# Kernel tuning notes

Measured on AMD Instinct MI355X. Metric: run time of the kernel, lower is better.

## Reference

```python
import jax, jax.numpy as jnp
import numpy as np

B, T, IN, H, OUT = 32, 1024, 256, 768, 128


def setup_inputs() -> dict:
    key = jax.random.key(0)
    ks = jax.random.split(key, 11)
    s = 0.05
    return {
        "x": jax.random.normal(ks[0], (B, T, IN), dtype=jnp.float32),
        "W_ih0": jax.random.normal(ks[1], (4 * H, IN), dtype=jnp.float32) * s,
        "W_hh0": jax.random.normal(ks[2], (4 * H, H), dtype=jnp.float32) * s,
        "b_ih0": jax.random.normal(ks[3], (4 * H,), dtype=jnp.float32) * s,
        "b_hh0": jax.random.normal(ks[4], (4 * H,), dtype=jnp.float32) * s,
        "W_ih1": jax.random.normal(ks[5], (4 * H, H), dtype=jnp.float32) * s,
        "W_hh1": jax.random.normal(ks[6], (4 * H, H), dtype=jnp.float32) * s,
        "b_ih1": jax.random.normal(ks[7], (4 * H,), dtype=jnp.float32) * s,
        "b_hh1": jax.random.normal(ks[8], (4 * H,), dtype=jnp.float32) * s,
        "W_lin": jax.random.normal(ks[9], (OUT, H), dtype=jnp.float32) * s,
        "b_lin": jax.random.normal(ks[10], (OUT,), dtype=jnp.float32) * s,
    }


def _lstm_layer(x_btd, W_ih, W_hh, b_ih, b_hh):
    # Input-side GEMM for all timesteps at once: [B,T,4H]
    xg = jnp.einsum("btd,gd->btg", x_btd, W_ih) + b_ih + b_hh
    xg = jnp.swapaxes(xg, 0, 1)  # time-major [T,B,4H]
    h0 = jnp.zeros((x_btd.shape[0], W_hh.shape[1]), x_btd.dtype)

    def step(carry, gx):
        h, c = carry
        g = gx + h @ W_hh.T  # [B,4H]
        i, f, gg, o = jnp.split(g, 4, axis=-1)  # PyTorch gate order i,f,g,o
        i, f, o = jax.nn.sigmoid(i), jax.nn.sigmoid(f), jax.nn.sigmoid(o)
        c = f * c + i * jnp.tanh(gg)
        h = o * jnp.tanh(c)
        return (h, c), h

    _, hs = jax.lax.scan(step, (h0, h0), xg)  # hs: [T,B,H]
    return jnp.swapaxes(hs, 0, 1)  # [B,T,H]


def reference(x, W_ih0, W_hh0, b_ih0, b_hh0, W_ih1, W_hh1, b_ih1, b_hh1, W_lin, b_lin):
    h1 = _lstm_layer(x, W_ih0, W_hh0, b_ih0, b_hh0)
    h2 = _lstm_layer(h1, W_ih1, W_hh1, b_ih1, b_hh1)  # eval mode: inter-layer dropout off
    return jnp.einsum("bth,oh->bto", h2, W_lin) + b_lin
```

## Files before the change

kernel.cpp:

```cpp
#include <hip/hip_runtime.h>

#define Tt    1024
#define INF   256
#define Hh    768
#define OUTF  128

#define NWG_L0  48
#define NWG_L1  48
#define NWG_LIN 2
#define NWG     (NWG_L0 + NWG_L1 + NWG_LIN)
#define NTHR    1024

typedef unsigned int       u32;
typedef unsigned long long u64;
typedef unsigned short     u16;
typedef __attribute__((ext_vector_type(8))) short bf16x8;
typedef __attribute__((ext_vector_type(4))) float f32x4;

#define PROG_OFF 0
#define HA_OFF   16384
#define HB_OFF   (HA_OFF + 3*49152)
#define WS_BYTES (HB_OFF + 3*49152)
#define HPS      24576

#define ASTR_B 1552
#define RSLAB  272
#define RROW   17

__device__ __forceinline__ float sigf(float v){ return 1.0f/(1.0f+__expf(-v)); }
__device__ __forceinline__ float tanhfast(float x){
    const float cx = fminf(fmaxf(x, -15.f), 15.f);
    const float e  = __expf(2.f * cx);
    return (e - 1.f) / (e + 1.f);
}
__device__ __forceinline__ u16 f2bf(float f){
    u32 u = __float_as_uint(f);
    return (u16)((u + 0x7fffu + ((u>>16)&1u)) >> 16);
}
__device__ __forceinline__ void st32ws(u16* p, u32 v){
    __hip_atomic_store((u32*)p, v, __ATOMIC_RELAXED, __HIP_MEMORY_SCOPE_AGENT);
}
__device__ __forceinline__ u32 ldu32(const u32* p){
    return __hip_atomic_load(p, __ATOMIC_RELAXED, __HIP_MEMORY_SCOPE_AGENT);
}
__device__ __forceinline__ void stu32(u32* p, u32 v){
    __hip_atomic_store(p, v, __ATOMIC_RELAXED, __HIP_MEMORY_SCOPE_AGENT);
}
__device__ __forceinline__ void ld16x3(const u16* p0, const u16* p1, const u16* p2,
                                       f32x4& r0, f32x4& r1, f32x4& r2){
    asm volatile(
        "global_load_dwordx4 %0, %3, off sc0 sc1\n\t"
        "global_load_dwordx4 %1, %4, off sc0 sc1\n\t"
        "global_load_dwordx4 %2, %5, off sc0 sc1\n\t"
        "s_waitcnt vmcnt(0)"
        : "=&v"(r0), "=&v"(r1), "=&v"(r2)
        : "v"(p0), "v"(p1), "v"(p2)
        : "memory");
}
__device__ __forceinline__ void ld16x6(const u16* p0, const u16* p1, const u16* p2,
                                       const u16* p3, const u16* p4, const u16* p5,
                                       f32x4& r0, f32x4& r1, f32x4& r2,
                                       f32x4& r3, f32x4& r4, f32x4& r5){
    asm volatile(
        "global_load_dwordx4 %0, %6, off sc0 sc1\n\t"
        "global_load_dwordx4 %1, %7, off sc0 sc1\n\t"
        "global_load_dwordx4 %2, %8, off sc0 sc1\n\t"
        "global_load_dwordx4 %3, %9, off sc0 sc1\n\t"
        "global_load_dwordx4 %4, %10, off sc0 sc1\n\t"
        "global_load_dwordx4 %5, %11, off sc0 sc1\n\t"
        "s_waitcnt vmcnt(0)"
        : "=&v"(r0), "=&v"(r1), "=&v"(r2), "=&v"(r3), "=&v"(r4), "=&v"(r5)
        : "v"(p0), "v"(p1), "v"(p2), "v"(p3), "v"(p4), "v"(p5)
        : "memory");
}

__device__ __forceinline__ void waitlines(u32* prog, int base, int cnt, u32 thr, int lane){
    bool ok = (lane >= cnt);
    int guard = 0;
    while (guard < (1 << 24)) {
        if (!ok) ok = (ldu32(prog + (base + lane) * 32) >= thr);
        if (__ballot(ok) == ~0ull) break;
        __builtin_amdgcn_s_sleep(1);
        ++guard;
    }
}

__global__ void prologue(char* ws){
    int i = blockIdx.x * 256 + threadIdx.x;
    if (i < WS_BYTES / 4)
        __hip_atomic_store(((u32*)ws) + i, 0u, __ATOMIC_RELAXED, __HIP_MEMORY_SCOPE_AGENT);
}

__device__ __forceinline__ bf16x8 load8w(const float* p){
    float4 v0 = *(const float4*)(p);
    float4 v1 = *(const float4*)(p + 4);
    bf16x8 r;
    r[0]=(short)f2bf(v0.x); r[1]=(short)f2bf(v0.y); r[2]=(short)f2bf(v0.z); r[3]=(short)f2bf(v0.w);
    r[4]=(short)f2bf(v1.x); r[5]=(short)f2bf(v1.y); r[6]=(short)f2bf(v1.z); r[7]=(short)f2bf(v1.w);
    return r;
}

__global__ __launch_bounds__(NTHR) void lstm_persist(
    const float* __restrict__ x,
    const float* __restrict__ Wih0, const float* __restrict__ Whh0,
    const float* __restrict__ bih0, const float* __restrict__ bhh0,
    const float* __restrict__ Wih1, const float* __restrict__ Whh1,
    const float* __restrict__ bih1, const float* __restrict__ bhh1,
    const float* __restrict__ Wlin, const float* __restrict__ blin,
    float* __restrict__ out, char* ws)
{
    u32* prog = (u32*)(ws + PROG_OFF);
    u16* hA   = (u16*)(ws + HA_OFF);
    u16* hB   = (u16*)(ws + HB_OFF);

    const int wg  = blockIdx.x;
    const int tid = threadIdx.x;

    __shared__ __align__(16) char smem[49664];
    char*  actb = smem;
    float* red  = (float*)smem;

    const int lane = tid & 63, w = tid >> 6;
    const int quad = lane >> 4, nl = lane & 15;
    const int nt = w >> 2, ks = w & 3;
    const int b3 = tid >> 5, q = tid & 31;

    const int role  = (wg < NWG_L0) ? 0 : ((wg < NWG_L0 + NWG_L1) ? 1 : 2);
    const int jbase = (role == 0) ? wg * 16 : ((role == 1) ? (wg - NWG_L0) * 16 : 0);
    const int obase = (role == 2) ? (wg - NWG_L0 - NWG_L1) * 64 : 0;

    bf16x8 bfr[12];
    if (role == 0) {
        const int grow = nt * Hh + jbase + nl;
        #pragma unroll
        for (int fi = 0; fi < 8; ++fi) {
            const int c = fi >> 2, fc = fi & 3;
            const int ka = c * 512 + ks * 128 + fc * 32 + quad * 8;
            const float* p = (ka < 256) ? (Wih0 + (size_t)grow * 256 + ka)
                                        : (Whh0 + (size_t)grow * 768 + (ka - 256));
            bfr[fi] = load8w(p);
        }
    } else if (role == 1) {
        const int grow = nt * Hh + jbase + nl;
        #pragma unroll
        for (int fi = 0; fi < 12; ++fi) {
            const int c = fi / 6, fc = fi % 6;
            const int ka = c * 768 + ks * 192 + fc * 32 + quad * 8;
            const float* p = (ka < 768) ? (Wih1 + (size_t)grow * 768 + ka)
                                        : (Whh1 + (size_t)grow * 768 + (ka - 768));
            bfr[fi] = load8w(p);
        }
    } else {
        const int row = obase + nt * 16 + nl;
        #pragma unroll
        for (int fi = 0; fi < 6; ++fi) {
            const int ka = ks * 192 + fi * 32 + quad * 8;
            bfr[fi] = load8w(Wlin + (size_t)row * 768 + ka);
        }
    }

    float ba0=0,ba1=0,ba2=0,ba3=0, bb0=0,bb1=0,bb2=0,bb3=0, creg0=0, creg1=0;
    float bl0 = 0.f, bl1 = 0.f;
    if (role < 2 && tid < 256) {
        const int jg0 = jbase + 2 * (tid >> 5), jg1 = jg0 + 1;
        const float* bi = (role == 0) ? bih0 : bih1;
        const float* bh = (role == 0) ? bhh0 : bhh1;
        ba0 = bi[jg0]        + bh[jg0];        bb0 = bi[jg1]        + bh[jg1];
        ba1 = bi[768 + jg0]  + bh[768 + jg0];  bb1 = bi[768 + jg1]  + bh[768 + jg1];
        ba2 = bi[1536 + jg0] + bh[1536 + jg0]; bb2 = bi[1536 + jg1] + bh[1536 + jg1];
        ba3 = bi[2304 + jg0] + bh[2304 + jg0]; bb3 = bi[2304 + jg1] + bh[2304 + jg1];
    }
    if (role == 2) {
        bl0 = blin[obase + (tid >> 5)];
        bl1 = blin[obase + 32 + (tid >> 5)];
    }

    for (int s = 0; s < Tt + 2; ++s) {
        const bool active = (role == 0) ? (s < Tt)
                          : (role == 1) ? (s >= 1 && s <= Tt)
                          :               (s >= 2);
        const int par_wA = s % 3;
        const int par_rA = (s + 2) % 3;
        const int par_wB = (s + 2) % 3;
        const int par_rB = (s + 1) % 3;

        if (active && w == 0) {
            if (role == 0) {
                if (s >= 1) waitlines(prog, 0, 48, (u32)s, lane);
                if (s >= 2) waitlines(prog, 48, 48, (u32)(s - 1), lane);
            } else if (role == 1) {
                waitlines(prog, 48, 48, (u32)s, lane);
                {
                    const u32 thr2 = (lane < 48) ? (u32)s : (u32)(s - 1);
                    const int idx  = (lane < 48) ? lane : (96 + (lane - 48));
                    bool ok = (lane >= 50);
                    int guard = 0;
                    while (guard < (1 << 24)) {
                        if (!ok) ok = (ldu32(prog + idx * 32) >= thr2);
                        if (__ballot(ok) == ~0ull) break;
                        __builtin_amdgcn_s_sleep(1);
                        ++guard;
                    }
                }
            } else {
                waitlines(prog, 48, 48, (u32)s, lane);
            }
        }
        __syncthreads();

        if (active) {
            f32x4 acc0 = {0.f,0.f,0.f,0.f}, acc1 = {0.f,0.f,0.f,0.f};

            if (role == 0) {
                const float* xs = x + ((size_t)b3 * Tt + s) * INF + q * 8;
                const float4 v0 = *(const float4*)xs;
                const float4 v1 = *(const float4*)(xs + 4);
                const u16* hp = hA + (size_t)par_rA * HPS + b3 * 768;
                f32x4 h0, h1, h2;
                ld16x3(hp + q * 8, hp + 256 + q * 8, hp + 512 + q * 8, h0, h1, h2);
                {
                    uint4 xv;
                    xv.x = (u32)f2bf(v0.x) | ((u32)f2bf(v0.y) << 16);
                    xv.y = (u32)f2bf(v0.z) | ((u32)f2bf(v0.w) << 16);
                    xv.z = (u32)f2bf(v1.x) | ((u32)f2bf(v1.y) << 16);
                    xv.w = (u32)f2bf(v1.z) | ((u32)f2bf(v1.w) << 16);
                    *(uint4*)(actb + b3 * ASTR_B + q * 16) = xv;
                    *(f32x4*)(actb + b3 * ASTR_B + 512 + q * 16) = h0;
                }
                __syncthreads();
                #pragma unroll
                for (int fc = 0; fc < 4; ++fc) {
                    const int koff = ks * 128 + fc * 32 + quad * 8;
                    bf16x8 a0 = *(const bf16x8*)(actb + nl * ASTR_B + koff * 2);
                    bf16x8 a1 = *(const bf16x8*)(actb + (16 + nl) * ASTR_B + koff * 2);
                    acc0 = __builtin_amdgcn_mfma_f32_16x16x32_bf16(a0, bfr[fc], acc0, 0, 0, 0);
                    acc1 = __builtin_amdgcn_mfma_f32_16x16x32_bf16(a1, bfr[fc], acc1, 0, 0, 0);
                }
                __syncthreads();
                *(f32x4*)(actb + b3 * ASTR_B + q * 16)       = h1;
                *(f32x4*)(actb + b3 * ASTR_B + 512 + q * 16) = h2;
                __syncthreads();
                #pragma unroll
                for (int fc = 0; fc < 4; ++fc) {
                    const int koff = ks * 128 + fc * 32 + quad * 8;
                    bf16x8 a0 = *(const bf16x8*)(actb + nl * ASTR_B + koff * 2);
                    bf16x8 a1 = *(const bf16x8*)(actb + (16 + nl) * ASTR_B + koff * 2);
                    acc0 = __builtin_amdgcn_mfma_f32_16x16x32_bf16(a0, bfr[4 + fc], acc0, 0, 0, 0);
                    acc1 = __builtin_amdgcn_mfma_f32_16x16x32_bf16(a1, bfr[4 + fc], acc1, 0, 0, 0);
                }
                __syncthreads();
            } else if (role == 1) {
                const u16* pA = hA + (size_t)par_rA * HPS + b3 * 768;
                const u16* pB = hB + (size_t)par_rB * HPS + b3 * 768;
                f32x4 a0, a1, a2, bq0, bq1, bq2;
                ld16x6(pA + q * 8, pA + 256 + q * 8, pA + 512 + q * 8,
                       pB + q * 8, pB + 256 + q * 8, pB + 512 + q * 8,
                       a0, a1, a2, bq0, bq1, bq2);
                *(f32x4*)(actb + b3 * ASTR_B + q * 16)        = a0;
                *(f32x4*)(actb + b3 * ASTR_B + 512 + q * 16)  = a1;
                *(f32x4*)(actb + b3 * ASTR_B + 1024 + q * 16) = a2;
                __syncthreads();
                #pragma unroll
                for (int fc = 0; fc < 6; ++fc) {
                    const int koff = ks * 192 + fc * 32 + quad * 8;
                    bf16x8 f0 = *(const bf16x8*)(actb + nl * ASTR_B + koff * 2);
                    bf16x8 f1 = *(const bf16x8*)(actb + (16 + nl) * ASTR_B + koff * 2);
                    acc0 = __builtin_amdgcn_mfma_f32_16x16x32_bf16(f0, bfr[fc], acc0, 0, 0, 0);
                    acc1 = __builtin_amdgcn_mfma_f32_16x16x32_bf16(f1, bfr[fc], acc1, 0, 0, 0);
                }
                __syncthreads();
                *(f32x4*)(actb + b3 * ASTR_B + q * 16)        = bq0;
                *(f32x4*)(actb + b3 * ASTR_B + 512 + q * 16)  = bq1;
                *(f32x4*)(actb + b3 * ASTR_B + 1024 + q * 16) = bq2;
                __syncthreads();
                #pragma unroll
                for (int fc = 0; fc < 6; ++fc) {
                    const int koff = ks * 192 + fc * 32 + quad * 8;
                    bf16x8 f0 = *(const bf16x8*)(actb + nl * ASTR_B + koff * 2);
                    bf16x8 f1 = *(const bf16x8*)(actb + (16 + nl) * ASTR_B + koff * 2);
                    acc0 = __builtin_amdgcn_mfma_f32_16x16x32_bf16(f0, bfr[6 + fc], acc0, 0, 0, 0);
                    acc1 = __builtin_amdgcn_mfma_f32_16x16x32_bf16(f1, bfr[6 + fc], acc1, 0, 0, 0);
                }
                __syncthreads();
            } else {
                const u16* pB = hB + (size_t)par_rB * HPS + b3 * 768;
                f32x4 bq0, bq1, bq2;
                ld16x3(pB + q * 8, pB + 256 + q * 8, pB + 512 + q * 8, bq0, bq1, bq2);
                *(f32x4*)(actb + b3 * ASTR_B + q * 16)        = bq0;
                *(f32x4*)(actb + b3 * ASTR_B + 512 + q * 16)  = bq1;
                *(f32x4*)(actb + b3 * ASTR_B + 1024 + q * 16) = bq2;
                __syncthreads();
                #pragma unroll
                for (int fc = 0; fc < 6; ++fc) {
                    const int koff = ks * 192 + fc * 32 + quad * 8;
                    bf16x8 f0 = *(const bf16x8*)(actb + nl * ASTR_B + koff * 2);
                    bf16x8 f1 = *(const bf16x8*)(actb + (16 + nl) * ASTR_B + koff * 2);
                    acc0 = __builtin_amdgcn_mfma_f32_16x16x32_bf16(f0, bfr[fc], acc0, 0, 0, 0);
                    acc1 = __builtin_amdgcn_mfma_f32_16x16x32_bf16(f1, bfr[fc], acc1, 0, 0, 0);
                }
                __syncthreads();
            }

            *(f32x4*)(red + (size_t)((nt * 2 + 0) * 4 + ks) * RSLAB + nl * RROW + quad * 4) = acc0;
            *(f32x4*)(red + (size_t)((nt * 2 + 1) * 4 + ks) * RSLAB + nl * RROW + quad * 4) = acc1;
            __syncthreads();

            if (role == 2) {
                const int r2 = tid >> 5, bb = tid & 31;
                const int mtr = bb >> 4, mr = bb & 15;
                const int nt0 = r2 >> 4, nr0 = r2 & 15;
                const int nt1 = (r2 + 32) >> 4, nr1 = (r2 + 32) & 15;
                float s0 = 0.f, s1 = 0.f;
                #pragma unroll
                for (int k2 = 0; k2 < 4; ++k2) {
                    s0 += red[(size_t)((nt0 * 2 + mtr) * 4 + k2) * RSLAB + nr0 * RROW + mr];
                    s1 += red[(size_t)((nt1 * 2 + mtr) * 4 + k2) * RSLAB + nr1 * RROW + mr];
                }
                const int v = s - 2;
                float* o = out + ((size_t)bb * Tt + v) * OUTF + obase;
                o[r2]      = s0 + bl0;
                o[32 + r2] = s1 + bl1;
            } else if (tid < 256) {
                const int jj = tid >> 5, b2 = tid & 31;
                const int mt = b2 >> 4, mr = b2 & 15;
                const int j0 = 2 * jj, j1 = 2 * jj + 1;
                float p0a=0,p1a=0,p2a=0,p3a=0, p0b=0,p1b=0,p2b=0,p3b=0;
                #pragma unroll
                for (int k2 = 0; k2 < 4; ++k2) {
                    p0a += red[(size_t)((0 * 2 + mt) * 4 + k2) * RSLAB + j0 * RROW + mr];
                    p1a += red[(size_t)((1 * 2 + mt) * 4 + k2) * RSLAB + j0 * RROW + mr];
                    p2a += red[(size_t)((2 * 2 + mt) * 4 + k2) * RSLAB + j0 * RROW + mr];
                    p3a += red[(size_t)((3 * 2 + mt) * 4 + k2) * RSLAB + j0 * RROW + mr];
                    p0b += red[(size_t)((0 * 2 + mt) * 4 + k2) * RSLAB + j1 * RROW + mr];
                    p1b += red[(size_t)((1 * 2 + mt) * 4 + k2) * RSLAB + j1 * RROW + mr];
                    p2b += red[(size_t)((2 * 2 + mt) * 4 + k2) * RSLAB + j1 * RROW + mr];
                    p3b += red[(size_t)((3 * 2 + mt) * 4 + k2) * RSLAB + j1 * RROW + mr];
                }
                const float ig0 = sigf(ba0 + p0a), fg0 = sigf(ba1 + p1a);
                const float gv0 = tanhfast(ba2 + p2a), og0 = sigf(ba3 + p3a);
                creg0 = fg0 * creg0 + ig0 * gv0;
                const float h0 = og0 * tanhfast(creg0);
                const float ig1 = sigf(bb0 + p0b), fg1 = sigf(bb1 + p1b);
                const float gv1 = tanhfast(bb2 + p2b), og1 = sigf(bb3 + p3b);
                creg1 = fg1 * creg1 + ig1 * gv1;
                const float h1 = og1 * tanhfast(creg1);
                u16* dst = (role == 0) ? (hA + (size_t)par_wA * HPS)
                                       : (hB + (size_t)par_wB * HPS);
                st32ws(dst + b2 * 768 + jbase + j0, (u32)f2bf(h0) | ((u32)f2bf(h1) << 16));
            }
        }

        __syncthreads();
        if (tid == 0) stu32(prog + wg * 32, (u32)(s + 1));
    }
}

extern "C" void kernel_launch(void* const* d_in, const int* in_sizes, int n_in,
                              void* d_out, int out_size, void* d_ws, size_t ws_size,
                              hipStream_t stream)
{
    const float* x    = (const float*)d_in[0];
    const float* Wih0 = (const float*)d_in[1];
    const float* Whh0 = (const float*)d_in[2];
    const float* bih0 = (const float*)d_in[3];
    const float* bhh0 = (const float*)d_in[4];
    const float* Wih1 = (const float*)d_in[5];
    const float* Whh1 = (const float*)d_in[6];
    const float* bih1 = (const float*)d_in[7];
    const float* bhh1 = (const float*)d_in[8];
    const float* Wlin = (const float*)d_in[9];
    const float* blin = (const float*)d_in[10];
    float* out = (float*)d_out;
    char*  ws  = (char*)d_ws;

    hipLaunchKernelGGL(prologue, dim3(304), dim3(256), 0, stream, ws);
    hipLaunchKernelGGL(lstm_persist, dim3(NWG), dim3(NTHR), 0, stream,
                       x, Wih0, Whh0, bih0, bhh0,
                       Wih1, Whh1, bih1, bhh1,
                       Wlin, blin, out, ws);
}
```

Before: 6.240 ms.

## Split batch into two independent half-batch streams interleaved across iterations

Each timestep is split into two half-batch iterations of 16 rows, so one half's recurrence can proceed while the other half's dependencies are still being published. The activation tile is staged once per iteration with an XOR-swizzled LDS layout, replacing the two-phase K staging and its extra barriers. Progress polling is spread over two waves. Per-iteration latency should drop, but the iteration count doubles, the MFMA per iteration halves, and the number of grid-wide flag synchronisations rises.

```diff
diff --git a/kernel.cpp b/kernel.cpp
--- a/kernel.cpp
+++ b/kernel.cpp
@@ -10,6 +10,7 @@
 #define NWG_LIN 2
 #define NWG     (NWG_L0 + NWG_L1 + NWG_LIN)
 #define NTHR    1024
+#define NIT     (2 * Tt + 4)
 
 typedef unsigned int       u32;
 typedef unsigned long long u64;
@@ -18,14 +19,16 @@
 typedef __attribute__((ext_vector_type(4))) float f32x4;
 
 #define PROG_OFF 0
+#define HPS16    12288
 #define HA_OFF   16384
-#define HB_OFF   (HA_OFF + 3*49152)
-#define WS_BYTES (HB_OFF + 3*49152)
-#define HPS      24576
-
-#define ASTR_B 1552
-#define RSLAB  272
-#define RROW   17
+#define HB_OFF   (HA_OFF + 6 * HPS16 * 2)
+#define WS_BYTES (HB_OFF + 6 * HPS16 * 2)
+
+#define AST0  2048
+#define AST1  3072
+#define AST2  1536
+#define RSLAB 272
+#define RROW  17
 
 __device__ __forceinline__ float sigf(float v){ return 1.0f/(1.0f+__expf(-v)); }
 __device__ __forceinline__ float tanhfast(float x){
@@ -46,31 +49,27 @@
 __device__ __forceinline__ void stu32(u32* p, u32 v){
     __hip_atomic_store(p, v, __ATOMIC_RELAXED, __HIP_MEMORY_SCOPE_AGENT);
 }
-__device__ __forceinline__ void ld16x3(const u16* p0, const u16* p1, const u16* p2,
-                                       f32x4& r0, f32x4& r1, f32x4& r2){
+__device__ __forceinline__ void ld16x2(const u16* p0, const u16* p1,
+                                       f32x4& r0, f32x4& r1){
     asm volatile(
-        "global_load_dwordx4 %0, %3, off sc0 sc1\n\t"
-        "global_load_dwordx4 %1, %4, off sc0 sc1\n\t"
-        "global_load_dwordx4 %2, %5, off sc0 sc1\n\t"
+        "global_load_dwordx4 %0, %2, off sc0 sc1\n\t"
+        "global_load_dwordx4 %1, %3, off sc0 sc1\n\t"
         "s_waitcnt vmcnt(0)"
-        : "=&v"(r0), "=&v"(r1), "=&v"(r2)
-        : "v"(p0), "v"(p1), "v"(p2)
+        : "=&v"(r0), "=&v"(r1)
+        : "v"(p0), "v"(p1)
         : "memory");
 }
-__device__ __forceinline__ void ld16x6(const u16* p0, const u16* p1, const u16* p2,
-                                       const u16* p3, const u16* p4, const u16* p5,
-                                       f32x4& r0, f32x4& r1, f32x4& r2,
-                                       f32x4& r3, f32x4& r4, f32x4& r5){
+__device__ __forceinline__ void ld16x4(const u16* p0, const u16* p1,
+                                       const u16* p2, const u16* p3,
+                                       f32x4& r0, f32x4& r1, f32x4& r2, f32x4& r3){
     asm volatile(
-        "global_load_dwordx4 %0, %6, off sc0 sc1\n\t"
-        "global_load_dwordx4 %1, %7, off sc0 sc1\n\t"
-        "global_load_dwordx4 %2, %8, off sc0 sc1\n\t"
-        "global_load_dwordx4 %3, %9, off sc0 sc1\n\t"
-        "global_load_dwordx4 %4, %10, off sc0 sc1\n\t"
-        "global_load_dwordx4 %5, %11, off sc0 sc1\n\t"
+        "global_load_dwordx4 %0, %4, off sc0 sc1\n\t"
+        "global_load_dwordx4 %1, %5, off sc0 sc1\n\t"
+        "global_load_dwordx4 %2, %6, off sc0 sc1\n\t"
+        "global_load_dwordx4 %3, %7, off sc0 sc1\n\t"
         "s_waitcnt vmcnt(0)"
-        : "=&v"(r0), "=&v"(r1), "=&v"(r2), "=&v"(r3), "=&v"(r4), "=&v"(r5)
-        : "v"(p0), "v"(p1), "v"(p2), "v"(p3), "v"(p4), "v"(p5)
+        : "=&v"(r0), "=&v"(r1), "=&v"(r2), "=&v"(r3)
+        : "v"(p0), "v"(p1), "v"(p2), "v"(p3)
         : "memory");
 }
 
@@ -116,26 +115,26 @@
     const int wg  = blockIdx.x;
     const int tid = threadIdx.x;
 
-    __shared__ __align__(16) char smem[49664];
-    char*  actb = smem;
-    float* red  = (float*)smem;
+    __shared__ __align__(16) char smem[50176];
 
     const int lane = tid & 63, w = tid >> 6;
     const int quad = lane >> 4, nl = lane & 15;
     const int nt = w >> 2, ks = w & 3;
-    const int b3 = tid >> 5, q = tid & 31;
+    const int srow = tid & 15, g2 = tid >> 4;
 
     const int role  = (wg < NWG_L0) ? 0 : ((wg < NWG_L0 + NWG_L1) ? 1 : 2);
     const int jbase = (role == 0) ? wg * 16 : ((role == 1) ? (wg - NWG_L0) * 16 : 0);
     const int obase = (role == 2) ? (wg - NWG_L0 - NWG_L1) * 64 : 0;
+
+    char*  actb = smem;
+    float* red  = (float*)(smem + ((role == 0) ? 32768 : (role == 1) ? 0 : 24576));
 
     bf16x8 bfr[12];
     if (role == 0) {
         const int grow = nt * Hh + jbase + nl;
         #pragma unroll
         for (int fi = 0; fi < 8; ++fi) {
-            const int c = fi >> 2, fc = fi & 3;
-            const int ka = c * 512 + ks * 128 + fc * 32 + quad * 8;
+            const int ka = ks * 256 + fi * 32 + quad * 8;
             const float* p = (ka < 256) ? (Wih0 + (size_t)grow * 256 + ka)
                                         : (Whh0 + (size_t)grow * 768 + (ka - 256));
             bfr[fi] = load8w(p);
@@ -144,8 +143,7 @@
         const int grow = nt * Hh + jbase + nl;
         #pragma unroll
         for (int fi = 0; fi < 12; ++fi) {
-            const int c = fi / 6, fc = fi % 6;
-            const int ka = c * 768 + ks * 192 + fc * 32 + quad * 8;
+            const int ka = ks * 384 + fi * 32 + quad * 8;
             const float* p = (ka < 768) ? (Wih1 + (size_t)grow * 768 + ka)
                                         : (Whh1 + (size_t)grow * 768 + (ka - 768));
             bfr[fi] = load8w(p);
@@ -159,10 +157,11 @@
         }
     }
 
-    float ba0=0,ba1=0,ba2=0,ba3=0, bb0=0,bb1=0,bb2=0,bb3=0, creg0=0, creg1=0;
-    float bl0 = 0.f, bl1 = 0.f;
-    if (role < 2 && tid < 256) {
-        const int jg0 = jbase + 2 * (tid >> 5), jg1 = jg0 + 1;
+    float ba0=0,ba1=0,ba2=0,ba3=0, bb0=0,bb1=0,bb2=0,bb3=0;
+    float c00=0, c01=0, c10=0, c11=0;
+    float bl = 0.f;
+    if (role < 2 && tid < 128) {
+        const int jg0 = jbase + 2 * (tid >> 4), jg1 = jg0 + 1;
         const float* bi = (role == 0) ? bih0 : bih1;
         const float* bh = (role == 0) ? bhh0 : bhh1;
         ba0 = bi[jg0]        + bh[jg0];        bb0 = bi[jg1]        + bh[jg1];
@@ -170,28 +169,24 @@
         ba2 = bi[1536 + jg0] + bh[1536 + jg0]; bb2 = bi[1536 + jg1] + bh[1536 + jg1];
         ba3 = bi[2304 + jg0] + bh[2304 + jg0]; bb3 = bi[2304 + jg1] + bh[2304 + jg1];
     }
-    if (role == 2) {
-        bl0 = blin[obase + (tid >> 5)];
-        bl1 = blin[obase + 32 + (tid >> 5)];
-    }
-
-    for (int s = 0; s < Tt + 2; ++s) {
-        const bool active = (role == 0) ? (s < Tt)
-                          : (role == 1) ? (s >= 1 && s <= Tt)
-                          :               (s >= 2);
-        const int par_wA = s % 3;
-        const int par_rA = (s + 2) % 3;
-        const int par_wB = (s + 2) % 3;
-        const int par_rB = (s + 1) % 3;
-
-        if (active && w == 0) {
+    if (role == 2) bl = blin[obase + (tid >> 4)];
+
+    for (int i = 0; i < NIT; ++i) {
+        const int t = i >> 1, half = i & 1;
+        const int pr0 = t % 3, pr1 = (t + 1) % 3, pr2 = (t + 2) % 3;
+        const bool active = (role == 0) ? (i < 2 * Tt)
+                          : (role == 1) ? (i >= 2 && i < 2 * Tt + 2)
+                          :               (i >= 4);
+
+        if (active) {
             if (role == 0) {
-                if (s >= 1) waitlines(prog, 0, 48, (u32)s, lane);
-                if (s >= 2) waitlines(prog, 48, 48, (u32)(s - 1), lane);
+                if (w == 0 && i >= 2) waitlines(prog, 0, 48, (u32)(i - 1), lane);
+                if (w == 1 && i >= 4) waitlines(prog, 48, 48, (u32)(i - 3), lane);
             } else if (role == 1) {
-                waitlines(prog, 48, 48, (u32)s, lane);
-                {
-                    const u32 thr2 = (lane < 48) ? (u32)s : (u32)(s - 1);
+                if (w == 0) waitlines(prog, 48, 48, (u32)(i - 1), lane);
+                if (w == 1) {
+                    const u32 thr2 = (lane < 48) ? (u32)(i - 1)
+                                                 : ((i >= 4) ? (u32)(i - 3) : 0u);
                     const int idx  = (lane < 48) ? lane : (96 + (lane - 48));
                     bool ok = (lane >= 50);
                     int guard = 0;
@@ -203,155 +198,147 @@
                     }
                 }
             } else {
-                waitlines(prog, 48, 48, (u32)s, lane);
+                if (w == 0) waitlines(prog, 48, 48, (u32)(i - 1), lane);
             }
         }
         __syncthreads();
 
         if (active) {
-            f32x4 acc0 = {0.f,0.f,0.f,0.f}, acc1 = {0.f,0.f,0.f,0.f};
-
+            const u32 swz = (u32)((srow & 7) << 4);
             if (role == 0) {
-                const float* xs = x + ((size_t)b3 * Tt + s) * INF + q * 8;
-                const float4 v0 = *(const float4*)xs;
-                const float4 v1 = *(const float4*)(xs + 4);
-                const u16* hp = hA + (size_t)par_rA * HPS + b3 * 768;
-                f32x4 h0, h1, h2;
-                ld16x3(hp + q * 8, hp + 256 + q * 8, hp + 512 + q * 8, h0, h1, h2);
-                {
-                    uint4 xv;
-                    xv.x = (u32)f2bf(v0.x) | ((u32)f2bf(v0.y) << 16);
-                    xv.y = (u32)f2bf(v0.z) | ((u32)f2bf(v0.w) << 16);
-                    xv.z = (u32)f2bf(v1.x) | ((u32)f2bf(v1.y) << 16);
-                    xv.w = (u32)f2bf(v1.z) | ((u32)f2bf(v1.w) << 16);
-                    *(uint4*)(actb + b3 * ASTR_B + q * 16) = xv;
-                    *(f32x4*)(actb + b3 * ASTR_B + 512 + q * 16) = h0;
-                }
-                __syncthreads();
-                #pragma unroll
-                for (int fc = 0; fc < 4; ++fc) {
-                    const int koff = ks * 128 + fc * 32 + quad * 8;
-                    bf16x8 a0 = *(const bf16x8*)(actb + nl * ASTR_B + koff * 2);
-                    bf16x8 a1 = *(const bf16x8*)(actb + (16 + nl) * ASTR_B + koff * 2);
-                    acc0 = __builtin_amdgcn_mfma_f32_16x16x32_bf16(a0, bfr[fc], acc0, 0, 0, 0);
-                    acc1 = __builtin_amdgcn_mfma_f32_16x16x32_bf16(a1, bfr[fc], acc1, 0, 0, 0);
-                }
-                __syncthreads();
-                *(f32x4*)(actb + b3 * ASTR_B + q * 16)       = h1;
-                *(f32x4*)(actb + b3 * ASTR_B + 512 + q * 16) = h2;
-                __syncthreads();
-                #pragma unroll
-                for (int fc = 0; fc < 4; ++fc) {
-                    const int koff = ks * 128 + fc * 32 + quad * 8;
-                    bf16x8 a0 = *(const bf16x8*)(actb + nl * ASTR_B + koff * 2);
-                    bf16x8 a1 = *(const bf16x8*)(actb + (16 + nl) * ASTR_B + koff * 2);
-                    acc0 = __builtin_amdgcn_mfma_f32_16x16x32_bf16(a0, bfr[4 + fc], acc0, 0, 0, 0);
-                    acc1 = __builtin_amdgcn_mfma_f32_16x16x32_bf16(a1, bfr[4 + fc], acc1, 0, 0, 0);
-                }
-                __syncthreads();
+                const u32 c0 = (u32)(srow * AST0 + g2 * 32);
+                if (g2 < 16) {
+                    const int trow = half * 16 + srow;
+                    const float* xs = x + ((size_t)trow * Tt + t) * INF + g2 * 16;
+                    const float4 v0 = ((const float4*)xs)[0];
+                    const float4 v1 = ((const float4*)xs)[1];
+                    const float4 v2 = ((const float4*)xs)[2];
+                    const float4 v3 = ((const float4*)xs)[3];
+                    uint4 a, b;
+                    a.x = (u32)f2bf(v0.x) | ((u32)f2bf(v0.y) << 16);
+                    a.y = (u32)f2bf(v0.z) | ((u32)f2bf(v0.w) << 16);
+                    a.z = (u32)f2bf(v1.x) | ((u32)f2bf(v1.y) << 16);
+                    a.w = (u32)f2bf(v1.z) | ((u32)f2bf(v1.w) << 16);
+                    b.x = (u32)f2bf(v2.x) | ((u32)f2bf(v2.y) << 16);
+                    b.y = (u32)f2bf(v2.z) | ((u32)f2bf(v2.w) << 16);
+                    b.z = (u32)f2bf(v3.x) | ((u32)f2bf(v3.y) << 16);
+                    b.w = (u32)f2bf(v3.z) | ((u32)f2bf(v3.w) << 16);
+                    *(uint4*)(actb + (c0 ^ swz))        = a;
+                    *(uint4*)(actb + ((c0 + 16) ^ swz)) = b;
+                } else {
+                    const u16* hp = hA + (size_t)(half * 3 + pr2) * HPS16
+                                       + srow * 768 + (g2 - 16) * 16;
+                    f32x4 r0, r1;
+                    ld16x2(hp, hp + 8, r0, r1);
+                    *(f32x4*)(actb + (c0 ^ swz))        = r0;
+                    *(f32x4*)(actb + ((c0 + 16) ^ swz)) = r1;
+                }
             } else if (role == 1) {
-                const u16* pA = hA + (size_t)par_rA * HPS + b3 * 768;
-                const u16* pB = hB + (size_t)par_rB * HPS + b3 * 768;
-                f32x4 a0, a1, a2, bq0, bq1, bq2;
-                ld16x6(pA + q * 8, pA + 256 + q * 8, pA + 512 + q * 8,
-                       pB + q * 8, pB + 256 + q * 8, pB + 512 + q * 8,
-                       a0, a1, a2, bq0, bq1, bq2);
-                *(f32x4*)(actb + b3 * ASTR_B + q * 16)        = a0;
-                *(f32x4*)(actb + b3 * ASTR_B + 512 + q * 16)  = a1;
-                *(f32x4*)(actb + b3 * ASTR_B + 1024 + q * 16) = a2;
-                __syncthreads();
+                const u16* pA = hA + (size_t)(half * 3 + pr2) * HPS16 + srow * 768;
+                const u16* pB = hB + (size_t)(half * 3 + pr1) * HPS16 + srow * 768;
+                if (g2 < 32) {
+                    const u16* p1 = pA + g2 * 16;
+                    const u16* p2 = pB + (g2 + 16) * 16;
+                    f32x4 r0, r1, r2, r3;
+                    ld16x4(p1, p1 + 8, p2, p2 + 8, r0, r1, r2, r3);
+                    const u32 c0 = (u32)(srow * AST1 + g2 * 32);
+                    const u32 c1 = (u32)(srow * AST1 + (g2 + 64) * 32);
+                    *(f32x4*)(actb + (c0 ^ swz))        = r0;
+                    *(f32x4*)(actb + ((c0 + 16) ^ swz)) = r1;
+                    *(f32x4*)(actb + (c1 ^ swz))        = r2;
+                    *(f32x4*)(actb + ((c1 + 16) ^ swz)) = r3;
+                } else {
+                    const u16* p1 = (g2 < 48) ? (pA + g2 * 16) : (pB + (g2 - 48) * 16);
+                    f32x4 r0, r1;
+                    ld16x2(p1, p1 + 8, r0, r1);
+                    const u32 c0 = (u32)(srow * AST1 + g2 * 32);
+                    *(f32x4*)(actb + (c0 ^ swz))        = r0;
+                    *(f32x4*)(actb + ((c0 + 16) ^ swz)) = r1;
+                }
+            } else {
+                if (tid < 768) {
+                    const u16* pB = hB + (size_t)(half * 3 + pr1) * HPS16
+                                       + srow * 768 + g2 * 16;
+                    f32x4 r0, r1;
+                    ld16x2(pB, pB + 8, r0, r1);
+                    const u32 c0 = (u32)(srow * AST2 + g2 * 32);
+                    *(f32x4*)(actb + (c0 ^ swz))        = r0;
+                    *(f32x4*)(actb + ((c0 + 16) ^ swz)) = r1;
+                }
+            }
+            __syncthreads();
+
+            f32x4 acc = {0.f, 0.f, 0.f, 0.f};
+            const u32 swzr = (u32)((nl & 7) << 4);
+            if (role == 0) {
+                #pragma unroll
+                for (int fc = 0; fc < 8; ++fc) {
+                    const u32 off = (u32)(nl * AST0 + (ks * 256 + fc * 32 + quad * 8) * 2);
+                    bf16x8 a = *(const bf16x8*)(actb + (off ^ swzr));
+                    acc = __builtin_amdgcn_mfma_f32_16x16x32_bf16(a, bfr[fc], acc, 0, 0, 0);
+                }
+            } else if (role == 1) {
+                #pragma unroll
+                for (int fc = 0; fc < 12; ++fc) {
+                    const u32 off = (u32)(nl * AST1 + (ks * 384 + fc * 32 + quad * 8) * 2);
+                    bf16x8 a = *(const bf16x8*)(actb + (off ^ swzr));
+                    acc = __builtin_amdgcn_mfma_f32_16x16x32_bf16(a, bfr[fc], acc, 0, 0, 0);
+                }
+            } else {
                 #pragma unroll
                 for (int fc = 0; fc < 6; ++fc) {
-                    const int koff = ks * 192 + fc * 32 + quad * 8;
-                    bf16x8 f0 = *(const bf16x8*)(actb + nl * ASTR_B + koff * 2);
-                    bf16x8 f1 = *(const bf16x8*)(actb + (16 + nl) * ASTR_B + koff * 2);
-                    acc0 = __builtin_amdgcn_mfma_f32_16x16x32_bf16(f0, bfr[fc], acc0, 0, 0, 0);
-                    acc1 = __builtin_amdgcn_mfma_f32_16x16x32_bf16(f1, bfr[fc], acc1, 0, 0, 0);
-                }
-                __syncthreads();
-                *(f32x4*)(actb + b3 * ASTR_B + q * 16)        = bq0;
-                *(f32x4*)(actb + b3 * ASTR_B + 512 + q * 16)  = bq1;
-                *(f32x4*)(actb + b3 * ASTR_B + 1024 + q * 16) = bq2;
-                __syncthreads();
-                #pragma unroll
-                for (int fc = 0; fc < 6; ++fc) {
-                    const int koff = ks * 192 + fc * 32 + quad * 8;
-                    bf16x8 f0 = *(const bf16x8*)(actb + nl * ASTR_B + koff * 2);
-                    bf16x8 f1 = *(const bf16x8*)(actb + (16 + nl) * ASTR_B + koff * 2);
-                    acc0 = __builtin_amdgcn_mfma_f32_16x16x32_bf16(f0, bfr[6 + fc], acc0, 0, 0, 0);
-                    acc1 = __builtin_amdgcn_mfma_f32_16x16x32_bf16(f1, bfr[6 + fc], acc1, 0, 0, 0);
-                }
-                __syncthreads();
-            } else {
-                const u16* pB = hB + (size_t)par_rB * HPS + b3 * 768;
-                f32x4 bq0, bq1, bq2;
-                ld16x3(pB + q * 8, pB + 256 + q * 8, pB + 512 + q * 8, bq0, bq1, bq2);
-                *(f32x4*)(actb + b3 * ASTR_B + q * 16)        = bq0;
-                *(f32x4*)(actb + b3 * ASTR_B + 512 + q * 16)  = bq1;
-                *(f32x4*)(actb + b3 * ASTR_B + 1024 + q * 16) = bq2;
-                __syncthreads();
-                #pragma unroll
-                for (int fc = 0; fc < 6; ++fc) {
-                    const int koff = ks * 192 + fc * 32 + quad * 8;
-                    bf16x8 f0 = *(const bf16x8*)(actb + nl * ASTR_B + koff * 2);
-                    bf16x8 f1 = *(const bf16x8*)(actb + (16 + nl) * ASTR_B + koff * 2);
-                    acc0 = __builtin_amdgcn_mfma_f32_16x16x32_bf16(f0, bfr[fc], acc0, 0, 0, 0);
-                    acc1 = __builtin_amdgcn_mfma_f32_16x16x32_bf16(f1, bfr[fc], acc1, 0, 0, 0);
-                }
-                __syncthreads();
+                    const u32 off = (u32)(nl * AST2 + (ks * 192 + fc * 32 + quad * 8) * 2);
+                    bf16x8 a = *(const bf16x8*)(actb + (off ^ swzr));
+                    acc = __builtin_amdgcn_mfma_f32_16x16x32_bf16(a, bfr[fc], acc, 0, 0, 0);
+                }
             }
-
-            *(f32x4*)(red + (size_t)((nt * 2 + 0) * 4 + ks) * RSLAB + nl * RROW + quad * 4) = acc0;
-            *(f32x4*)(red + (size_t)((nt * 2 + 1) * 4 + ks) * RSLAB + nl * RROW + quad * 4) = acc1;
+            if (role == 1) __syncthreads();
+            *(f32x4*)(red + (size_t)(nt * 4 + ks) * RSLAB + nl * RROW + quad * 4) = acc;
             __syncthreads();
 
             if (role == 2) {
-                const int r2 = tid >> 5, bb = tid & 31;
-                const int mtr = bb >> 4, mr = bb & 15;
-                const int nt0 = r2 >> 4, nr0 = r2 & 15;
-                const int nt1 = (r2 + 32) >> 4, nr1 = (r2 + 32) & 15;
-                float s0 = 0.f, s1 = 0.f;
+                const int lt = t - 2;
+                const int oc = tid >> 4, orow = tid & 15;
+                float ssum = bl;
+                #pragma unroll
+                for (int k2 = 0; k2 < 4; ++k2)
+                    ssum += red[(size_t)((oc >> 4) * 4 + k2) * RSLAB + (oc & 15) * RROW + orow];
+                out[((size_t)(half * 16 + orow) * Tt + lt) * OUTF + obase + oc] = ssum;
+            } else if (tid < 128) {
+                const int jj = tid >> 4, b2 = tid & 15;
+                const int j0 = 2 * jj, j1 = j0 + 1;
+                float p0a=0,p1a=0,p2a=0,p3a=0, p0b=0,p1b=0,p2b=0,p3b=0;
                 #pragma unroll
                 for (int k2 = 0; k2 < 4; ++k2) {
-                    s0 += red[(size_t)((nt0 * 2 + mtr) * 4 + k2) * RSLAB + nr0 * RROW + mr];
-                    s1 += red[(size_t)((nt1 * 2 + mtr) * 4 + k2) * RSLAB + nr1 * RROW + mr];
-                }
-                const int v = s - 2;
-                float* o = out + ((size_t)bb * Tt + v) * OUTF + obase;
-                o[r2]      = s0 + bl0;
-                o[32 + r2] = s1 + bl1;
-            } else if (tid < 256) {
-                const int jj = tid >> 5, b2 = tid & 31;
-                const int mt = b2 >> 4, mr = b2 & 15;
-                const int j0 = 2 * jj, j1 = 2 * jj + 1;
-                float p0a=0,p1a=0,p2a=0,p3a=0, p0b=0,p1b=0,p2b=0,p3b=0;
-                #pragma unroll
-                for (int k2 = 0; k2 < 4; ++k2) {
-                    p0a += red[(size_t)((0 * 2 + mt) * 4 + k2) * RSLAB + j0 * RROW + mr];
-                    p1a += red[(size_t)((1 * 2 + mt) * 4 + k2) * RSLAB + j0 * RROW + mr];
-                    p2a += red[(size_t)((2 * 2 + mt) * 4 + k2) * RSLAB + j0 * RROW + mr];
-                    p3a += red[(size_t)((3 * 2 + mt) * 4 + k2) * RSLAB + j0 * RROW + mr];
-                    p0b += red[(size_t)((0 * 2 + mt) * 4 + k2) * RSLAB + j1 * RROW + mr];
-                    p1b += red[(size_t)((1 * 2 + mt) * 4 + k2) * RSLAB + j1 * RROW + mr];
-                    p2b += red[(size_t)((2 * 2 + mt) * 4 + k2) * RSLAB + j1 * RROW + mr];
-                    p3b += red[(size_t)((3 * 2 + mt) * 4 + k2) * RSLAB + j1 * RROW + mr];
-                }
+                    p0a += red[(size_t)(0 * 4 + k2) * RSLAB + j0 * RROW + b2];
+                    p1a += red[(size_t)(1 * 4 + k2) * RSLAB + j0 * RROW + b2];
+                    p2a += red[(size_t)(2 * 4 + k2) * RSLAB + j0 * RROW + b2];
+                    p3a += red[(size_t)(3 * 4 + k2) * RSLAB + j0 * RROW + b2];
+                    p0b += red[(size_t)(0 * 4 + k2) * RSLAB + j1 * RROW + b2];
+                    p1b += red[(size_t)(1 * 4 + k2) * RSLAB + j1 * RROW + b2];
+                    p2b += red[(size_t)(2 * 4 + k2) * RSLAB + j1 * RROW + b2];
+                    p3b += red[(size_t)(3 * 4 + k2) * RSLAB + j1 * RROW + b2];
+                }
+                float cA = half ? c10 : c00;
+                float cB = half ? c11 : c01;
                 const float ig0 = sigf(ba0 + p0a), fg0 = sigf(ba1 + p1a);
                 const float gv0 = tanhfast(ba2 + p2a), og0 = sigf(ba3 + p3a);
-                creg0 = fg0 * creg0 + ig0 * gv0;
-                const float h0 = og0 * tanhfast(creg0);
+                cA = fg0 * cA + ig0 * gv0;
+                const float h0 = og0 * tanhfast(cA);
                 const float ig1 = sigf(bb0 + p0b), fg1 = sigf(bb1 + p1b);
                 const float gv1 = tanhfast(bb2 + p2b), og1 = sigf(bb3 + p3b);
-                creg1 = fg1 * creg1 + ig1 * gv1;
-                const float h1 = og1 * tanhfast(creg1);
-                u16* dst = (role == 0) ? (hA + (size_t)par_wA * HPS)
-                                       : (hB + (size_t)par_wB * HPS);
-                st32ws(dst + b2 * 768 + jbase + j0, (u32)f2bf(h0) | ((u32)f2bf(h1) << 16));
+                cB = fg1 * cB + ig1 * gv1;
+                const float h1 = og1 * tanhfast(cB);
+                if (half) { c10 = cA; c11 = cB; } else { c00 = cA; c01 = cB; }
+                const int parW = (role == 0) ? pr0 : pr2;
+                u16* dst = ((role == 0) ? hA : hB) + (size_t)(half * 3 + parW) * HPS16;
+                st32ws(dst + b2 * 768 + jbase + j0,
+                       (u32)f2bf(h0) | ((u32)f2bf(h1) << 16));
             }
         }
 
         __syncthreads();
-        if (tid == 0) stu32(prog + wg * 32, (u32)(s + 1));
+        if (tid == 0) stu32(prog + wg * 32, (u32)(i + 1));
     }
 }
 
```

Result: slower. 11.21 ms (+79.7%).
